# Kernel optimization log

Measured on AMD Instinct MI355X. Metric: run time of the kernel, lower is better.

Reference implementation:

```python
import jax, jax.numpy as jnp
import numpy as np

OBS_LEN = 20
N_COORD = 2
HIDDEN = 1024  # z_dim + c_dim = 512 + 512
N = 4096


def setup_inputs() -> dict:
    key = jax.random.key(0)
    ks = jax.random.split(key, 6)
    obs_traj_rel = jax.random.normal(ks[0], (OBS_LEN, N, N_COORD), dtype=jnp.float32)
    pred_lstm_hidden = jax.random.normal(ks[1], (N, HIDDEN), dtype=jnp.float32)
    # LSTMCell params (PyTorch layout): weight_ih [4H, in], weight_hh [4H, H],
    # initialized N(0, 0.1); biases zero (per _initialize_weights).
    W_ih = 0.1 * jax.random.normal(ks[2], (4 * HIDDEN, N_COORD), dtype=jnp.float32)
    W_hh = 0.1 * jax.random.normal(ks[3], (4 * HIDDEN, HIDDEN), dtype=jnp.float32)
    b_ih = jnp.zeros((4 * HIDDEN,), dtype=jnp.float32)
    b_hh = jnp.zeros((4 * HIDDEN,), dtype=jnp.float32)
    # hidden2pos Linear: weight [n_coord, H], bias zero
    W_out = 0.1 * jax.random.normal(ks[4], (N_COORD, HIDDEN), dtype=jnp.float32)
    b_out = jnp.zeros((N_COORD,), dtype=jnp.float32)
    return {
        "obs_traj_rel": obs_traj_rel,
        "pred_lstm_hidden": pred_lstm_hidden,
        "W_ih": W_ih,
        "W_hh": W_hh,
        "b_ih": b_ih,
        "b_hh": b_hh,
        "W_out": W_out,
        "b_out": b_out,
        "variant_feats": 1,
    }


def reference(obs_traj_rel, pred_lstm_hidden, W_ih, W_hh, b_ih, b_hh, W_out, b_out, variant_feats):
    # Step 0 consumes obs[0]; step i>=1 consumes obs[i-1] (per the original loop).
    x_seq = jnp.concatenate([obs_traj_rel[:1], obs_traj_rel[:-1]], axis=0)[..., :N_COORD]
    c0 = jnp.zeros_like(pred_lstm_hidden)

    def step(carry, x_t):
        h, c = carry
        # PyTorch LSTMCell: gates = x W_ih^T + b_ih + h W_hh^T + b_hh, order i,f,g,o
        gates = x_t @ W_ih.T + b_ih + h @ W_hh.T + b_hh
        i, f, g, o = jnp.split(gates, 4, axis=-1)
        c = jax.nn.sigmoid(f) * c + jax.nn.sigmoid(i) * jnp.tanh(g)
        h = jax.nn.sigmoid(o) * jnp.tanh(c)
        out = h @ W_out.T + b_out  # [N, n_coord]
        return (h, c), out

    _, outs = jax.lax.scan(step, (pred_lstm_hidden, c0), x_seq)
    return outs  # [obs_len, N, n_coord]
```

## Files before the change

### kernel.cpp

```cpp
#include <hip/hip_runtime.h>
#include <hip/hip_bf16.h>
#include <stdint.h>

#define N_BATCH 4096
#define HID     1024
#define OBSLEN  20

#define BM  256
#define BK  64

using short8 = __attribute__((ext_vector_type(8))) short;
using f32x4  = __attribute__((ext_vector_type(4))) float;

#define AS1 __attribute__((address_space(1)))
#define AS3 __attribute__((address_space(3)))

__device__ __forceinline__ float rcpf(float x) { return __builtin_amdgcn_rcpf(x); }
__device__ __forceinline__ float sigf(float x) { return rcpf(1.f + __expf(-x)); }
__device__ __forceinline__ float tanh_(float x) {
    float a = fminf(15.f, fmaxf(-15.f, x));
    float t = __expf(-2.f * a);
    return (1.f - t) * rcpf(1.f + t);
}
__device__ __forceinline__ unsigned short f2bf(float f) {
    __hip_bfloat16 b = __float2bfloat16(f);
    return *reinterpret_cast<unsigned short*>(&b);
}
__device__ __forceinline__ float bf2f(unsigned short u) {
    unsigned int x = ((unsigned int)u) << 16;
    return __uint_as_float(x);
}

__global__ __launch_bounds__(256) void prep_kernel(
    const float4* __restrict__ Whh, const float4* __restrict__ h0,
    ushort4* __restrict__ Wg, ushort4* __restrict__ hb, float4* __restrict__ c, int n4)
{
    int i = blockIdx.x * 256 + threadIdx.x;
    if (i < n4) {
        float4 h = h0[i];
        hb[i] = make_ushort4(f2bf(h.x), f2bf(h.y), f2bf(h.z), f2bf(h.w));
        c[i] = make_float4(0.f, 0.f, 0.f, 0.f);
        int R  = i >> 8, k4 = i & 255;
        int by = R >> 8, cp = R & 255;
        int g  = (cp >> 4) & 3;
        int hl = ((cp >> 6) << 4) | (cp & 15);
        int orig = g * HID + by * 64 + hl;
        float4 w = Whh[orig * 256 + k4];
        Wg[i] = make_ushort4(f2bf(w.x), f2bf(w.y), f2bf(w.z), f2bf(w.w));
    }
}

__global__ __launch_bounds__(512, 2) void lstm_step_kernel(
    const ushort* __restrict__ hin,
    const ushort* __restrict__ Wg,
    const float*  __restrict__ xt,
    const float*  __restrict__ Wih,
    const float*  __restrict__ bih,
    const float*  __restrict__ bhh,
    float*        __restrict__ cst,
    ushort*       __restrict__ hout)
{
    __shared__ __align__(16) char lds[131072];
    const int tid  = threadIdx.x;
    const int lane = tid & 63, l15 = lane & 15, l4 = lane >> 4;
    const int wid  = tid >> 6, wr = wid >> 2, wc = wid & 3;
    const int m0   = blockIdx.x * BM;
    const int by   = blockIdx.y;
    const int bid  = blockIdx.y * (N_BATCH / BM) + blockIdx.x;

    const int rowS = tid >> 3;
    const int offS = ((tid & 7) * 16) ^ ((rowS & 7) << 4);
    const ushort* aS = hin + (size_t)(m0 + rowS) * HID + (offS >> 1);
    const ushort* bS = Wg  + (size_t)(by * 256 + rowS) * HID + (offS >> 1);
    char* aD = lds + tid * 16;
    char* bD = lds + 65536 + tid * 16;

    auto stA = [&](int buf, int k0, int r) {
        __builtin_amdgcn_global_load_lds(
            (const AS1 void*)(aS + k0 + (size_t)r * 64 * HID),
            (AS3 void*)(aD + buf * 32768 + r * 8192), 16, 0, 0);
    };
    auto stB = [&](int buf, int k0, int r) {
        __builtin_amdgcn_global_load_lds(
            (const AS1 void*)(bS + k0 + (size_t)r * 64 * HID),
            (AS3 void*)(bD + buf * 32768 + r * 8192), 16, 0, 0);
    };

    const int swz   = (l15 & 7) << 4;
    const int kb0   = (l4 * 16) ^ swz;
    const int aBase = (wr * 128 + l15) * 128 + kb0;
    const int bBase = (wc * 64  + l15) * 128 + kb0;

    f32x4 acc[8][4];
#pragma unroll
    for (int f = 0; f < 8; ++f)
#pragma unroll
        for (int n = 0; n < 4; ++n)
            acc[f][n] = (f32x4){0.f, 0.f, 0.f, 0.f};

    stB(0, 0, 0); stB(0, 0, 1); stB(0, 0, 2); stB(0, 0, 3);
    stA(0, 0, 0); stA(0, 0, 2); stA(0, 0, 1); stA(0, 0, 3);

    short8 af[4], bfr[4];
    const int NK = HID / BK;
    for (int kt = 0; kt < NK; ++kt) {
        const int cur = kt & 1, nxt = cur ^ 1;
        const bool st = (kt < NK - 1);
        const int k1 = (kt + 1) * BK;
        const char* A = lds + cur * 32768;
        const char* B = lds + 65536 + cur * 32768;

        asm volatile("s_waitcnt vmcnt(2)" ::: "memory");
        __builtin_amdgcn_s_barrier();
        __builtin_amdgcn_sched_barrier(0);
#pragma unroll
        for (int f = 0; f < 4; ++f) af[f]  = *(const short8*)(A + aBase + f * 2048);
#pragma unroll
        for (int n = 0; n < 4; ++n) bfr[n] = *(const short8*)(B + bBase + n * 2048);
        if (st) { stB(nxt, k1, 0); stB(nxt, k1, 1); stB(nxt, k1, 2); }
        asm volatile("s_waitcnt lgkmcnt(0)" ::: "memory");
        __builtin_amdgcn_sched_barrier(0);
        __builtin_amdgcn_s_setprio(1);
#pragma unroll
        for (int f = 0; f < 4; ++f)
#pragma unroll
            for (int n = 0; n < 4; ++n)
                acc[f][n] = __builtin_amdgcn_mfma_f32_16x16x32_bf16(af[f], bfr[n], acc[f][n], 0, 0, 0);
        __builtin_amdgcn_s_setprio(0);

        if (st) asm volatile("s_waitcnt vmcnt(3)" ::: "memory");
        else    asm volatile("s_waitcnt vmcnt(0)" ::: "memory");
        __builtin_amdgcn_s_barrier();
        __builtin_amdgcn_sched_barrier(0);
#pragma unroll
        for (int f = 0; f < 4; ++f) af[f] = *(const short8*)(A + aBase + (f + 4) * 2048);
        if (st) { stB(nxt, k1, 3); stA(nxt, k1, 0); stA(nxt, k1, 2); }
        asm volatile("s_waitcnt lgkmcnt(0)" ::: "memory");
        __builtin_amdgcn_sched_barrier(0);
        __builtin_amdgcn_s_setprio(1);
#pragma unroll
        for (int f = 0; f < 4; ++f)
#pragma unroll
            for (int n = 0; n < 4; ++n)
                acc[f + 4][n] = __builtin_amdgcn_mfma_f32_16x16x32_bf16(af[f], bfr[n], acc[f + 4][n], 0, 0, 0);
        __builtin_amdgcn_s_setprio(0);

        __builtin_amdgcn_s_barrier();
        __builtin_amdgcn_sched_barrier(0);
#pragma unroll
        for (int f = 0; f < 4; ++f) af[f]  = *(const short8*)(A + (aBase ^ 64) + f * 2048);
#pragma unroll
        for (int n = 0; n < 4; ++n) bfr[n] = *(const short8*)(B + (bBase ^ 64) + n * 2048);
        if (st) { stA(nxt, k1, 1); stA(nxt, k1, 3); }
        asm volatile("s_waitcnt lgkmcnt(0)" ::: "memory");
        __builtin_amdgcn_sched_barrier(0);
        __builtin_amdgcn_s_setprio(1);
#pragma unroll
        for (int f = 0; f < 4; ++f)
#pragma unroll
            for (int n = 0; n < 4; ++n)
                acc[f][n] = __builtin_amdgcn_mfma_f32_16x16x32_bf16(af[f], bfr[n], acc[f][n], 0, 0, 0);
        __builtin_amdgcn_s_setprio(0);

        __builtin_amdgcn_s_barrier();
        __builtin_amdgcn_sched_barrier(0);
#pragma unroll
        for (int f = 0; f < 4; ++f) af[f] = *(const short8*)(A + (aBase ^ 64) + (f + 4) * 2048);
        asm volatile("s_waitcnt lgkmcnt(0)" ::: "memory");
        __builtin_amdgcn_sched_barrier(0);
        __builtin_amdgcn_s_setprio(1);
#pragma unroll
        for (int f = 0; f < 4; ++f)
#pragma unroll
            for (int n = 0; n < 4; ++n)
                acc[f + 4][n] = __builtin_amdgcn_mfma_f32_16x16x32_bf16(af[f], bfr[n], acc[f + 4][n], 0, 0, 0);
        __builtin_amdgcn_s_setprio(0);
    }

    float4* c4 = (float4*)cst + (size_t)bid * 4096;
    float4 cv[8];
#pragma unroll
    for (int f = 0; f < 8; ++f) cv[f] = c4[f * 512 + tid];

    const int hcg = by * 64 + wc * 16 + l15;
    float wi0[4], wi1[4], bs_[4];
#pragma unroll
    for (int n = 0; n < 4; ++n) {
        int j = n * HID + hcg;
        wi0[n] = Wih[j * 2 + 0];
        wi1[n] = Wih[j * 2 + 1];
        bs_[n] = bih[j] + bhh[j];
    }
    const float2* xt2 = (const float2*)xt;
#pragma unroll
    for (int f = 0; f < 8; ++f) {
#pragma unroll
        for (int r = 0; r < 4; ++r) {
            int nrow = m0 + wr * 128 + f * 16 + l4 * 4 + r;
            float2 x = xt2[nrow];
            float gi = acc[f][0][r] + x.x * wi0[0] + x.y * wi1[0] + bs_[0];
            float gf = acc[f][1][r] + x.x * wi0[1] + x.y * wi1[1] + bs_[1];
            float gg = acc[f][2][r] + x.x * wi0[2] + x.y * wi1[2] + bs_[2];
            float go = acc[f][3][r] + x.x * wi0[3] + x.y * wi1[3] + bs_[3];
            float iv = sigf(gi), fv = sigf(gf);
            float gv = tanh_(gg), ov = sigf(go);
            float cn = fv * cv[f][r] + iv * gv;
            cv[f][r] = cn;
            hout[(size_t)nrow * HID + hcg] = f2bf(ov * tanh_(cn));
        }
        c4[f * 512 + tid] = cv[f];
    }
}

__global__ __launch_bounds__(256) void out_proj_kernel(
    const ushort* __restrict__ h, const float* __restrict__ Wout,
    const float* __restrict__ bout, float* __restrict__ outt)
{
    const int wid = threadIdx.x >> 6, lane = threadIdx.x & 63;
    const int row = blockIdx.x * 4 + wid;
    const ushort* hr = h + (size_t)row * HID + lane * 16;
    float a0 = 0.f, a1 = 0.f;
#pragma unroll
    for (int half = 0; half < 2; ++half) {
        short8 hv = *(const short8*)(hr + half * 8);
#pragma unroll
        for (int j = 0; j < 8; ++j) {
            int k = lane * 16 + half * 8 + j;
            float f = bf2f((unsigned short)hv[j]);
            a0 += f * Wout[k];
            a1 += f * Wout[HID + k];
        }
    }
#pragma unroll
    for (int off = 32; off > 0; off >>= 1) {
        a0 += __shfl_down(a0, off);
        a1 += __shfl_down(a1, off);
    }
    if (lane == 0) {
        outt[row * 2 + 0] = a0 + bout[0];
        outt[row * 2 + 1] = a1 + bout[1];
    }
}

extern "C" void kernel_launch(void* const* d_in, const int* in_sizes, int n_in,
                              void* d_out, int out_size, void* d_ws, size_t ws_size,
                              hipStream_t stream) {
    const float* obs  = (const float*)d_in[0];
    const float* h0   = (const float*)d_in[1];
    const float* Wih  = (const float*)d_in[2];
    const float* Whh  = (const float*)d_in[3];
    const float* bih  = (const float*)d_in[4];
    const float* bhh  = (const float*)d_in[5];
    const float* Wout = (const float*)d_in[6];
    const float* bout = (const float*)d_in[7];
    float* out = (float*)d_out;

    char* ws = (char*)d_ws;
    ushort* Wg = (ushort*)(ws);
    ushort* hA = (ushort*)(ws + (8  << 20));
    ushort* hB = (ushort*)(ws + (16 << 20));
    float*  c  = (float* )(ws + (24 << 20));

    prep_kernel<<<4096, 256, 0, stream>>>((const float4*)Whh, (const float4*)h0,
                                          (ushort4*)Wg, (ushort4*)hA, (float4*)c,
                                          N_BATCH * HID / 4);

    ushort* hin = hA;
    ushort* hou = hB;
    for (int t = 0; t < OBSLEN; ++t) {
        const float* xt = obs + (size_t)(t == 0 ? 0 : (t - 1)) * N_BATCH * 2;
        lstm_step_kernel<<<dim3(N_BATCH / BM, (4 * HID) / 256), 512, 0, stream>>>(
            hin, Wg, xt, Wih, bih, bhh, c, hou);
        out_proj_kernel<<<N_BATCH / 4, 256, 0, stream>>>(
            hou, Wout, bout, out + (size_t)t * N_BATCH * 2);
        ushort* tmp = hin; hin = hou; hou = tmp;
    }
}
```

Baseline: 861.0 us.

## Restructure GEMM main loop into eight-phase pipeline with finer-grained async stages

```diff
diff --git a/kernel.cpp b/kernel.cpp
--- a/kernel.cpp
+++ b/kernel.cpp
@@ -70,26 +70,26 @@
 
     const int rowS = tid >> 3;
     const int offS = ((tid & 7) * 16) ^ ((rowS & 7) << 4);
-    const ushort* aS = hin + (size_t)(m0 + rowS) * HID + (offS >> 1);
-    const ushort* bS = Wg  + (size_t)(by * 256 + rowS) * HID + (offS >> 1);
-    char* aD = lds + tid * 16;
-    char* bD = lds + 65536 + tid * 16;
-
-    auto stA = [&](int buf, int k0, int r) {
+    const ushort* aS  = hin + (size_t)(m0 + rowS) * HID + (offS >> 1);
+    const ushort* bS2 = Wg + (size_t)(by * 256 + rowS + (rowS & 32)) * HID + (offS >> 1);
+    char* aDb = lds + tid * 16;
+    char* bDb = lds + 65536 + tid * 16 + (rowS & 32) * 128;
+
+    auto stA = [&](int s, int k0, int h, int r) {
         __builtin_amdgcn_global_load_lds(
-            (const AS1 void*)(aS + k0 + (size_t)r * 64 * HID),
-            (AS3 void*)(aD + buf * 32768 + r * 8192), 16, 0, 0);
+            (const AS1 void*)(aS + k0 + (size_t)(h * 64 + r * 128) * HID),
+            (AS3 void*)(aDb + s * 32768 + (h * 64 + r * 128) * 128), 16, 0, 0);
     };
-    auto stB = [&](int buf, int k0, int r) {
+    auto stB = [&](int s, int k0, int g, int r) {
         __builtin_amdgcn_global_load_lds(
-            (const AS1 void*)(bS + k0 + (size_t)r * 64 * HID),
-            (AS3 void*)(bD + buf * 32768 + r * 8192), 16, 0, 0);
+            (const AS1 void*)(bS2 + k0 + (size_t)(g * 32 + r * 128) * HID),
+            (AS3 void*)(bDb + s * 32768 + (g * 32 + r * 128) * 128), 16, 0, 0);
     };
 
-    const int swz   = (l15 & 7) << 4;
-    const int kb0   = (l4 * 16) ^ swz;
-    const int aBase = (wr * 128 + l15) * 128 + kb0;
-    const int bBase = (wc * 64  + l15) * 128 + kb0;
+    const int swz = (l15 & 7) << 4;
+    const int kb0 = (l4 * 16) ^ swz;
+    const int aRd = (wr * 128 + l15) * 128 + kb0;
+    const int bRd = 65536 + (wc * 64 + l15) * 128 + kb0;
 
     f32x4 acc[8][4];
 #pragma unroll
@@ -98,83 +98,78 @@
         for (int n = 0; n < 4; ++n)
             acc[f][n] = (f32x4){0.f, 0.f, 0.f, 0.f};
 
-    stB(0, 0, 0); stB(0, 0, 1); stB(0, 0, 2); stB(0, 0, 3);
-    stA(0, 0, 0); stA(0, 0, 2); stA(0, 0, 1); stA(0, 0, 3);
-
-    short8 af[4], bfr[4];
-    const int NK = HID / BK;
-    for (int kt = 0; kt < NK; ++kt) {
-        const int cur = kt & 1, nxt = cur ^ 1;
-        const bool st = (kt < NK - 1);
-        const int k1 = (kt + 1) * BK;
-        const char* A = lds + cur * 32768;
-        const char* B = lds + 65536 + cur * 32768;
-
-        asm volatile("s_waitcnt vmcnt(2)" ::: "memory");
-        __builtin_amdgcn_s_barrier();
-        __builtin_amdgcn_sched_barrier(0);
-#pragma unroll
-        for (int f = 0; f < 4; ++f) af[f]  = *(const short8*)(A + aBase + f * 2048);
-#pragma unroll
-        for (int n = 0; n < 4; ++n) bfr[n] = *(const short8*)(B + bBase + n * 2048);
-        if (st) { stB(nxt, k1, 0); stB(nxt, k1, 1); stB(nxt, k1, 2); }
-        asm volatile("s_waitcnt lgkmcnt(0)" ::: "memory");
-        __builtin_amdgcn_sched_barrier(0);
-        __builtin_amdgcn_s_setprio(1);
-#pragma unroll
-        for (int f = 0; f < 4; ++f)
-#pragma unroll
-            for (int n = 0; n < 4; ++n)
-                acc[f][n] = __builtin_amdgcn_mfma_f32_16x16x32_bf16(af[f], bfr[n], acc[f][n], 0, 0, 0);
-        __builtin_amdgcn_s_setprio(0);
-
-        if (st) asm volatile("s_waitcnt vmcnt(3)" ::: "memory");
-        else    asm volatile("s_waitcnt vmcnt(0)" ::: "memory");
-        __builtin_amdgcn_s_barrier();
-        __builtin_amdgcn_sched_barrier(0);
-#pragma unroll
-        for (int f = 0; f < 4; ++f) af[f] = *(const short8*)(A + aBase + (f + 4) * 2048);
-        if (st) { stB(nxt, k1, 3); stA(nxt, k1, 0); stA(nxt, k1, 2); }
-        asm volatile("s_waitcnt lgkmcnt(0)" ::: "memory");
-        __builtin_amdgcn_sched_barrier(0);
-        __builtin_amdgcn_s_setprio(1);
-#pragma unroll
-        for (int f = 0; f < 4; ++f)
-#pragma unroll
-            for (int n = 0; n < 4; ++n)
-                acc[f + 4][n] = __builtin_amdgcn_mfma_f32_16x16x32_bf16(af[f], bfr[n], acc[f + 4][n], 0, 0, 0);
-        __builtin_amdgcn_s_setprio(0);
-
-        __builtin_amdgcn_s_barrier();
-        __builtin_amdgcn_sched_barrier(0);
-#pragma unroll
-        for (int f = 0; f < 4; ++f) af[f]  = *(const short8*)(A + (aBase ^ 64) + f * 2048);
-#pragma unroll
-        for (int n = 0; n < 4; ++n) bfr[n] = *(const short8*)(B + (bBase ^ 64) + n * 2048);
-        if (st) { stA(nxt, k1, 1); stA(nxt, k1, 3); }
-        asm volatile("s_waitcnt lgkmcnt(0)" ::: "memory");
-        __builtin_amdgcn_sched_barrier(0);
-        __builtin_amdgcn_s_setprio(1);
-#pragma unroll
-        for (int f = 0; f < 4; ++f)
-#pragma unroll
-            for (int n = 0; n < 4; ++n)
-                acc[f][n] = __builtin_amdgcn_mfma_f32_16x16x32_bf16(af[f], bfr[n], acc[f][n], 0, 0, 0);
-        __builtin_amdgcn_s_setprio(0);
-
-        __builtin_amdgcn_s_barrier();
-        __builtin_amdgcn_sched_barrier(0);
-#pragma unroll
-        for (int f = 0; f < 4; ++f) af[f] = *(const short8*)(A + (aBase ^ 64) + (f + 4) * 2048);
-        asm volatile("s_waitcnt lgkmcnt(0)" ::: "memory");
-        __builtin_amdgcn_sched_barrier(0);
-        __builtin_amdgcn_s_setprio(1);
-#pragma unroll
-        for (int f = 0; f < 4; ++f)
-#pragma unroll
-            for (int n = 0; n < 4; ++n)
-                acc[f + 4][n] = __builtin_amdgcn_mfma_f32_16x16x32_bf16(af[f], bfr[n], acc[f + 4][n], 0, 0, 0);
-        __builtin_amdgcn_s_setprio(0);
+    short8 af0[4], af1[4], bf0_[2], bf1_[2];
+
+#define VM8 asm volatile("s_waitcnt vmcnt(8)" ::: "memory")
+#define VM6 asm volatile("s_waitcnt vmcnt(6)" ::: "memory")
+#define VM4 asm volatile("s_waitcnt vmcnt(4)" ::: "memory")
+#define VM0 asm volatile("s_waitcnt vmcnt(0)" ::: "memory")
+#define NOPW ((void)0)
+
+#define PHASE(S, FH, NH, DO_A, STAGE_STMT, END_WAIT)                               \
+    {                                                                              \
+        if (DO_A) {                                                                \
+            _Pragma("unroll") for (int f = 0; f < 4; ++f) {                        \
+                const int o = aRd + (S) * 32768 + ((FH) * 4 + f) * 2048;           \
+                af0[f] = *(const short8*)(lds + o);                                \
+                af1[f] = *(const short8*)(lds + (o ^ 64));                         \
+            }                                                                      \
+        }                                                                          \
+        _Pragma("unroll") for (int n = 0; n < 2; ++n) {                            \
+            const int o = bRd + (S) * 32768 + ((NH) * 2 + n) * 2048;               \
+            bf0_[n] = *(const short8*)(lds + o);                                   \
+            bf1_[n] = *(const short8*)(lds + (o ^ 64));                            \
+        }                                                                          \
+        STAGE_STMT;                                                                \
+        __builtin_amdgcn_s_barrier();                                              \
+        asm volatile("s_waitcnt lgkmcnt(0)" ::: "memory");                         \
+        __builtin_amdgcn_sched_barrier(0);                                         \
+        __builtin_amdgcn_s_setprio(1);                                             \
+        _Pragma("unroll") for (int f = 0; f < 4; ++f)                              \
+            _Pragma("unroll") for (int n = 0; n < 2; ++n) {                        \
+                acc[(FH)*4+f][(NH)*2+n] = __builtin_amdgcn_mfma_f32_16x16x32_bf16( \
+                    af0[f], bf0_[n], acc[(FH)*4+f][(NH)*2+n], 0, 0, 0);            \
+                acc[(FH)*4+f][(NH)*2+n] = __builtin_amdgcn_mfma_f32_16x16x32_bf16( \
+                    af1[f], bf1_[n], acc[(FH)*4+f][(NH)*2+n], 0, 0, 0);            \
+            }                                                                      \
+        __builtin_amdgcn_s_setprio(0);                                             \
+        END_WAIT;                                                                  \
+        __builtin_amdgcn_sched_barrier(0);                                         \
+        __builtin_amdgcn_s_barrier();                                              \
+    }
+
+    stA(0, 0, 0, 0);  stA(0, 0, 0, 1);
+    stB(0, 0, 0, 0);  stB(0, 0, 0, 1);
+    stA(0, 0, 1, 0);  stA(0, 0, 1, 1);
+    stB(0, 0, 1, 0);  stB(0, 0, 1, 1);
+    stA(1, 64, 0, 0); stA(1, 64, 0, 1);
+    stB(1, 64, 0, 0); stB(1, 64, 0, 1);
+    VM8;
+    __builtin_amdgcn_s_barrier();
+
+    for (int i = 0; i < 7; ++i) {
+        const int kb1 = (2 * i + 1) * 64;
+        const int kn0 = (2 * i + 2) * 64;
+        const int kn1 = (2 * i + 3) * 64;
+        PHASE(0, 0, 0, 1, (stA(1, kb1, 1, 0), stA(1, kb1, 1, 1)), VM6);
+        PHASE(0, 0, 1, 0, (stB(1, kb1, 1, 0), stB(1, kb1, 1, 1)), NOPW);
+        PHASE(0, 1, 0, 1, (stA(0, kn0, 0, 0), stA(0, kn0, 0, 1)), NOPW);
+        PHASE(0, 1, 1, 0, (stB(0, kn0, 0, 0), stB(0, kn0, 0, 1)), VM8);
+        PHASE(1, 0, 0, 1, (stA(0, kn0, 1, 0), stA(0, kn0, 1, 1)), VM6);
+        PHASE(1, 0, 1, 0, (stB(0, kn0, 1, 0), stB(0, kn0, 1, 1)), NOPW);
+        PHASE(1, 1, 0, 1, (stA(1, kn1, 0, 0), stA(1, kn1, 0, 1)), NOPW);
+        PHASE(1, 1, 1, 0, (stB(1, kn1, 0, 0), stB(1, kn1, 0, 1)), VM8);
+    }
+    {
+        const int kb1 = 15 * 64;
+        PHASE(0, 0, 0, 1, (stA(1, kb1, 1, 0), stA(1, kb1, 1, 1)), VM6);
+        PHASE(0, 0, 1, 0, (stB(1, kb1, 1, 0), stB(1, kb1, 1, 1)), NOPW);
+        PHASE(0, 1, 0, 1, NOPW, NOPW);
+        PHASE(0, 1, 1, 0, NOPW, VM4);
+        PHASE(1, 0, 0, 1, NOPW, VM0);
+        PHASE(1, 0, 1, 0, NOPW, NOPW);
+        PHASE(1, 1, 0, 1, NOPW, NOPW);
+        PHASE(1, 1, 1, 0, NOPW, NOPW);
     }
 
     float4* c4 = (float4*)cst + (size_t)bid * 4096;
@@ -210,6 +205,12 @@
         }
         c4[f * 512 + tid] = cv[f];
     }
+#undef PHASE
+#undef VM8
+#undef VM6
+#undef VM4
+#undef VM0
+#undef NOPW
 }
 
 __global__ __launch_bounds__(256) void out_proj_kernel(
```

New measurement: 900.0 us. +4.5%, slower.

## Register double-buffer MFMA operands, cut barriers, and remap blocks per XCD

Applied to the files above, without the earlier changes.

```diff
diff --git a/kernel.cpp b/kernel.cpp
--- a/kernel.cpp
+++ b/kernel.cpp
@@ -64,9 +64,14 @@
     const int tid  = threadIdx.x;
     const int lane = tid & 63, l15 = lane & 15, l4 = lane >> 4;
     const int wid  = tid >> 6, wr = wid >> 2, wc = wid & 3;
-    const int m0   = blockIdx.x * BM;
-    const int by   = blockIdx.y;
-    const int bid  = blockIdx.y * (N_BATCH / BM) + blockIdx.x;
+
+    const int L    = blockIdx.x + (int)gridDim.x * blockIdx.y;
+    const int xcd  = L & 7, slot = L >> 3;
+    const int xb   = slot & 15;
+    const int yb   = (xcd << 1) | (slot >> 4);
+    const int m0   = xb * BM;
+    const int by   = yb;
+    const int bid  = yb * 16 + xb;
 
     const int rowS = tid >> 3;
     const int offS = ((tid & 7) * 16) ^ ((rowS & 7) << 4);
@@ -75,21 +80,21 @@
     char* aD = lds + tid * 16;
     char* bD = lds + 65536 + tid * 16;
 
-    auto stA = [&](int buf, int k0, int r) {
+    auto stA = [&](int s, int k0, int r) {
         __builtin_amdgcn_global_load_lds(
             (const AS1 void*)(aS + k0 + (size_t)r * 64 * HID),
-            (AS3 void*)(aD + buf * 32768 + r * 8192), 16, 0, 0);
+            (AS3 void*)(aD + s * 32768 + r * 8192), 16, 0, 0);
     };
-    auto stB = [&](int buf, int k0, int r) {
+    auto stB = [&](int s, int k0, int r) {
         __builtin_amdgcn_global_load_lds(
             (const AS1 void*)(bS + k0 + (size_t)r * 64 * HID),
-            (AS3 void*)(bD + buf * 32768 + r * 8192), 16, 0, 0);
+            (AS3 void*)(bD + s * 32768 + r * 8192), 16, 0, 0);
     };
 
-    const int swz   = (l15 & 7) << 4;
-    const int kb0   = (l4 * 16) ^ swz;
-    const int aBase = (wr * 128 + l15) * 128 + kb0;
-    const int bBase = (wc * 64  + l15) * 128 + kb0;
+    const int swz = (l15 & 7) << 4;
+    const int kb0 = (l4 * 16) ^ swz;
+    const int aRd = (wr * 128 + l15) * 128 + kb0;
+    const int bRd = 65536 + (wc * 64 + l15) * 128 + kb0;
 
     f32x4 acc[8][4];
 #pragma unroll
@@ -98,82 +103,79 @@
         for (int n = 0; n < 4; ++n)
             acc[f][n] = (f32x4){0.f, 0.f, 0.f, 0.f};
 
-    stB(0, 0, 0); stB(0, 0, 1); stB(0, 0, 2); stB(0, 0, 3);
-    stA(0, 0, 0); stA(0, 0, 2); stA(0, 0, 1); stA(0, 0, 3);
-
-    short8 af[4], bfr[4];
+    short8 af_cur[4], af_nxt[4], bf_cur[4], bf_nxt[4];
+
+#pragma unroll
+    for (int r = 0; r < 4; ++r) stA(0, 0, r);
+#pragma unroll
+    for (int r = 0; r < 4; ++r) stB(0, 0, r);
+#pragma unroll
+    for (int r = 0; r < 4; ++r) stA(1, 64, r);
+    __syncthreads();
+#pragma unroll
+    for (int f = 0; f < 4; ++f) af_cur[f] = *(const short8*)(lds + aRd + f * 2048);
+#pragma unroll
+    for (int n = 0; n < 4; ++n) bf_cur[n] = *(const short8*)(lds + bRd + n * 2048);
+
     const int NK = HID / BK;
     for (int kt = 0; kt < NK; ++kt) {
-        const int cur = kt & 1, nxt = cur ^ 1;
-        const bool st = (kt < NK - 1);
-        const int k1 = (kt + 1) * BK;
-        const char* A = lds + cur * 32768;
-        const char* B = lds + 65536 + cur * 32768;
-
-        asm volatile("s_waitcnt vmcnt(2)" ::: "memory");
-        __builtin_amdgcn_s_barrier();
-        __builtin_amdgcn_sched_barrier(0);
-#pragma unroll
-        for (int f = 0; f < 4; ++f) af[f]  = *(const short8*)(A + aBase + f * 2048);
-#pragma unroll
-        for (int n = 0; n < 4; ++n) bfr[n] = *(const short8*)(B + bBase + n * 2048);
-        if (st) { stB(nxt, k1, 0); stB(nxt, k1, 1); stB(nxt, k1, 2); }
-        asm volatile("s_waitcnt lgkmcnt(0)" ::: "memory");
-        __builtin_amdgcn_sched_barrier(0);
-        __builtin_amdgcn_s_setprio(1);
-#pragma unroll
-        for (int f = 0; f < 4; ++f)
-#pragma unroll
-            for (int n = 0; n < 4; ++n)
-                acc[f][n] = __builtin_amdgcn_mfma_f32_16x16x32_bf16(af[f], bfr[n], acc[f][n], 0, 0, 0);
-        __builtin_amdgcn_s_setprio(0);
-
-        if (st) asm volatile("s_waitcnt vmcnt(3)" ::: "memory");
-        else    asm volatile("s_waitcnt vmcnt(0)" ::: "memory");
-        __builtin_amdgcn_s_barrier();
-        __builtin_amdgcn_sched_barrier(0);
-#pragma unroll
-        for (int f = 0; f < 4; ++f) af[f] = *(const short8*)(A + aBase + (f + 4) * 2048);
-        if (st) { stB(nxt, k1, 3); stA(nxt, k1, 0); stA(nxt, k1, 2); }
-        asm volatile("s_waitcnt lgkmcnt(0)" ::: "memory");
-        __builtin_amdgcn_sched_barrier(0);
-        __builtin_amdgcn_s_setprio(1);
-#pragma unroll
-        for (int f = 0; f < 4; ++f)
-#pragma unroll
-            for (int n = 0; n < 4; ++n)
-                acc[f + 4][n] = __builtin_amdgcn_mfma_f32_16x16x32_bf16(af[f], bfr[n], acc[f + 4][n], 0, 0, 0);
-        __builtin_amdgcn_s_setprio(0);
-
-        __builtin_amdgcn_s_barrier();
-        __builtin_amdgcn_sched_barrier(0);
-#pragma unroll
-        for (int f = 0; f < 4; ++f) af[f]  = *(const short8*)(A + (aBase ^ 64) + f * 2048);
-#pragma unroll
-        for (int n = 0; n < 4; ++n) bfr[n] = *(const short8*)(B + (bBase ^ 64) + n * 2048);
-        if (st) { stA(nxt, k1, 1); stA(nxt, k1, 3); }
-        asm volatile("s_waitcnt lgkmcnt(0)" ::: "memory");
-        __builtin_amdgcn_sched_barrier(0);
-        __builtin_amdgcn_s_setprio(1);
-#pragma unroll
-        for (int f = 0; f < 4; ++f)
-#pragma unroll
-            for (int n = 0; n < 4; ++n)
-                acc[f][n] = __builtin_amdgcn_mfma_f32_16x16x32_bf16(af[f], bfr[n], acc[f][n], 0, 0, 0);
-        __builtin_amdgcn_s_setprio(0);
-
-        __builtin_amdgcn_s_barrier();
-        __builtin_amdgcn_sched_barrier(0);
-#pragma unroll
-        for (int f = 0; f < 4; ++f) af[f] = *(const short8*)(A + (aBase ^ 64) + (f + 4) * 2048);
-        asm volatile("s_waitcnt lgkmcnt(0)" ::: "memory");
-        __builtin_amdgcn_sched_barrier(0);
-        __builtin_amdgcn_s_setprio(1);
-#pragma unroll
-        for (int f = 0; f < 4; ++f)
-#pragma unroll
-            for (int n = 0; n < 4; ++n)
-                acc[f + 4][n] = __builtin_amdgcn_mfma_f32_16x16x32_bf16(af[f], bfr[n], acc[f + 4][n], 0, 0, 0);
+        const int s = kt & 1, s1 = s ^ 1;
+        const int aB = s * 32768 + aRd;
+        const int bB = s * 32768 + bRd;
+
+        if (kt < NK - 1) {
+#pragma unroll
+            for (int r = 0; r < 4; ++r) stB(s1, (kt + 1) * BK, r);
+        }
+#pragma unroll
+        for (int f = 0; f < 4; ++f) af_nxt[f] = *(const short8*)(lds + aB + (f + 4) * 2048);
+#pragma unroll
+        for (int n = 0; n < 4; ++n) bf_nxt[n] = *(const short8*)(lds + ((bB + n * 2048) ^ 64));
+        __builtin_amdgcn_s_setprio(1);
+#pragma unroll
+        for (int f = 0; f < 4; ++f)
+#pragma unroll
+            for (int n = 0; n < 4; ++n)
+                acc[f][n] = __builtin_amdgcn_mfma_f32_16x16x32_bf16(af_cur[f], bf_cur[n], acc[f][n], 0, 0, 0);
+        __builtin_amdgcn_s_setprio(0);
+
+#pragma unroll
+        for (int f = 0; f < 4; ++f) af_cur[f] = *(const short8*)(lds + ((aB + f * 2048) ^ 64));
+        __builtin_amdgcn_s_setprio(1);
+#pragma unroll
+        for (int f = 0; f < 4; ++f)
+#pragma unroll
+            for (int n = 0; n < 4; ++n)
+                acc[f + 4][n] = __builtin_amdgcn_mfma_f32_16x16x32_bf16(af_nxt[f], bf_cur[n], acc[f + 4][n], 0, 0, 0);
+        __builtin_amdgcn_s_setprio(0);
+
+#pragma unroll
+        for (int f = 0; f < 4; ++f) af_nxt[f] = *(const short8*)(lds + ((aB + (f + 4) * 2048) ^ 64));
+        __builtin_amdgcn_s_setprio(1);
+#pragma unroll
+        for (int f = 0; f < 4; ++f)
+#pragma unroll
+            for (int n = 0; n < 4; ++n)
+                acc[f][n] = __builtin_amdgcn_mfma_f32_16x16x32_bf16(af_cur[f], bf_nxt[n], acc[f][n], 0, 0, 0);
+        __builtin_amdgcn_s_setprio(0);
+        __syncthreads();
+
+        if (kt < NK - 2) {
+#pragma unroll
+            for (int r = 0; r < 4; ++r) stA(s, (kt + 2) * BK, r);
+        }
+        if (kt < NK - 1) {
+#pragma unroll
+            for (int f = 0; f < 4; ++f) af_cur[f] = *(const short8*)(lds + s1 * 32768 + aRd + f * 2048);
+#pragma unroll
+            for (int n = 0; n < 4; ++n) bf_cur[n] = *(const short8*)(lds + s1 * 32768 + bRd + n * 2048);
+        }
+        __builtin_amdgcn_s_setprio(1);
+#pragma unroll
+        for (int f = 0; f < 4; ++f)
+#pragma unroll
+            for (int n = 0; n < 4; ++n)
+                acc[f + 4][n] = __builtin_amdgcn_mfma_f32_16x16x32_bf16(af_nxt[f], bf_nxt[n], acc[f + 4][n], 0, 0, 0);
         __builtin_amdgcn_s_setprio(0);
     }
 
```

Measured after the change: 868.9 us. About the same (+0.9%).
